# Performance work log

Measured on AMD Instinct MI355X. Metric: run time of the kernel, lower is better.

Reference implementation:

```python
import jax, jax.numpy as jnp
import numpy as np

# Config (matches init_kwargs): range [-32,32]^3, voxel 0.5 -> 128^3 grid; BEV 200x200
PC_LOW = np.array([-32.0, -32.0, -32.0], dtype=np.float32)
PC_HIGH = np.array([32.0, 32.0, 32.0], dtype=np.float32)
VOX = 0.5
G = 128
BEV_H, BEV_W = 200, 200
BN_EPS = 1e-5
STRIDES = [1, 2, 1, 2, 1, 1]


def setup_inputs() -> dict:
    key = jax.random.key(0)
    ks = jax.random.split(key, 10)
    N = 2_000_000
    xyz = jax.random.uniform(ks[0], (N, 3), jnp.float32, minval=-32.0, maxval=32.0)
    inten = jax.random.uniform(ks[1], (N, 1), jnp.float32)
    points = jnp.concatenate([xyz, inten], axis=1)  # (N,4)
    chans = [(32, 4), (64, 32), (64, 64), (128, 64), (128, 128), (256, 128)]
    inp = {"points": points}
    for i, (co, ci) in enumerate(chans):
        fan_in = ci * 27
        inp[f"w{i+1}"] = jax.random.normal(ks[2 + i], (co, ci, 3, 3, 3), jnp.float32) / np.sqrt(fan_in)
        inp[f"g{i+1}"] = jnp.ones((co,), jnp.float32)
        inp[f"b{i+1}"] = jnp.zeros((co,), jnp.float32)
    return inp


def _voxelize(points):
    # range filtering + floor-binning + clamp, faithful to voxelize_points (dense path: scatter-ADD)
    low = jnp.asarray(PC_LOW)
    high = jnp.asarray(PC_HIGH)
    mask = jnp.all((points[:, :3] >= low) & (points[:, :3] <= high), axis=1)
    coords = jnp.floor((points[:, :3] - low) / VOX).astype(jnp.int32)
    coords = jnp.clip(coords, 0, G - 1)
    vals = points * mask[:, None].astype(points.dtype)  # invalid points contribute 0
    # original indexes voxel_grid[:, z, y, x]
    grid = jnp.zeros((G, G, G, 4), points.dtype)
    grid = grid.at[coords[:, 2], coords[:, 1], coords[:, 0]].add(vals)
    return jnp.transpose(grid, (3, 0, 1, 2))  # (4, G, G, G)


def _conv3d(x, w, s):
    # PyTorch Conv3d(k=3, padding=1, stride=s), NCDHW
    return jax.lax.conv_general_dilated(
        x, w, window_strides=(s, s, s), padding=[(1, 1), (1, 1), (1, 1)],
        dimension_numbers=("NCDHW", "OIDHW", "NCDHW"))


def _bn_relu(x, g, b):
    # eval-mode BN: running_mean=0, running_var=1
    scale = (g / jnp.sqrt(1.0 + BN_EPS))[None, :, None, None, None]
    return jax.nn.relu(x * scale + b[None, :, None, None, None])


def reference(points, w1, w2, w3, w4, w5, w6,
              g1, g2, g3, g4, g5, g6,
              b1, b2, b3, b4, b5, b6):
    ws = [w1, w2, w3, w4, w5, w6]
    gs = [g1, g2, g3, g4, g5, g6]
    bs = [b1, b2, b3, b4, b5, b6]
    x = _voxelize(points)[None]  # (1,4,G,G,G)
    for w, g, b, s in zip(ws, gs, bs, STRIDES):
        x = _bn_relu(_conv3d(x, w, s), g, b)
    feat = x[0]  # (256, G/4, G/4, G/4)
    bev = jnp.max(feat, axis=2)  # torch.max(..., dim=2) on (C,D1,D2,D3) -> (C,D1,D3)
    # F.interpolate bilinear align_corners=False == jax.image.resize half-pixel bilinear
    bev = jax.image.resize(bev, (bev.shape[0], BEV_H, BEV_W), method="bilinear")
    return bev
```

## Files before the change

kernel.cpp:

```cpp
#include <hip/hip_runtime.h>
#include <hip/hip_fp16.h>
#include <cstdint>
#include <cstddef>

typedef __attribute__((ext_vector_type(8))) short short8;
typedef __attribute__((ext_vector_type(8))) _Float16 half8;
typedef __attribute__((ext_vector_type(16))) float f32x16;

__device__ __forceinline__ float bf2f(unsigned short u) { return __uint_as_float(((unsigned)u) << 16); }
__device__ __forceinline__ unsigned short f2bf(float f) {
    unsigned u = __float_as_uint(f);
    return (unsigned short)((u + 0x7fffu + ((u >> 16) & 1u)) >> 16);
}
__device__ __forceinline__ void sync_lds() {
    asm volatile("s_waitcnt lgkmcnt(0)\n\ts_barrier" ::: "memory");
}

static constexpr float BN_INV = 0.9999950000374997f;

__global__ __launch_bounds__(256) void voxelize_kernel(const float4* __restrict__ pts,
                                                       __half2* __restrict__ grid, int N) {
    int i = blockIdx.x * 256 + threadIdx.x;
    if (i >= N) return;
    float4 p = pts[i];
    if (p.x < -32.f || p.x > 32.f || p.y < -32.f || p.y > 32.f || p.z < -32.f || p.z > 32.f) return;
    int cx = min(max((int)floorf((p.x + 32.f) * 2.f), 0), 127);
    int cy = min(max((int)floorf((p.y + 32.f) * 2.f), 0), 127);
    int cz = min(max((int)floorf((p.z + 32.f) * 2.f), 0), 127);
    int idx = ((((cz + 1) * 130) + (cy + 1)) * 130 + (cx + 1)) * 2;
    unsafeAtomicAdd(&grid[idx],     __floats2half2_rn(p.x, p.y));
    unsafeAtomicAdd(&grid[idx + 1], __floats2half2_rn(p.z, p.w));
}

__global__ __launch_bounds__(256) void repack_w(const float* __restrict__ w, const float* __restrict__ g,
                                                unsigned short* __restrict__ o, int Co, int CI) {
    int i = blockIdx.x * 256 + threadIdx.x;
    int total = 27 * Co * CI;
    if (i >= total) return;
    int ci = i % CI;
    int t = i / CI;
    int co = t % Co;
    int k = t / Co;
    float v = w[((size_t)(co * CI + ci)) * 27 + k] * g[co] * BN_INV;
    o[i] = f2bf(v);
}
__global__ __launch_bounds__(256) void repack_w1m(const float* __restrict__ w, const float* __restrict__ g,
                                                  unsigned short* __restrict__ o) {
    int i = blockIdx.x * 256 + threadIdx.x;
    if (i >= 9 * 32 * 16) return;
    int k16 = i & 15;
    int co = (i >> 4) & 31;
    int p = i >> 9;
    float v = 0.f;
    if (k16 < 12) {
        int dx = k16 >> 2, ci = k16 & 3;
        int dz = p / 3, dy = p % 3;
        v = w[(co * 4 + ci) * 27 + dz * 9 + dy * 3 + dx] * g[co] * BN_INV;
    }
    o[i] = __half_as_ushort(__float2half(v));
}

__global__ __launch_bounds__(256) void conv1_mfma(
    const unsigned short* __restrict__ in, const unsigned short* __restrict__ wa,
    const float* __restrict__ beta, unsigned short* __restrict__ out,
    int zstart, int r0) {
    const int tid = threadIdx.x;
    const int l31 = tid & 31;
    const int lh = (tid >> 5) & 1;
    const int wv = tid >> 6;
    int v = blockIdx.x * 128 + wv * 32 + l31;
    int x = v & 127;
    int y = (v >> 7) & 127;
    int z = zstart + (v >> 14);

    const unsigned short* base = in + ((z * 130 + y) * 130 + x) * 4 + lh * 8;
    uint2 d0[9], d1[9];
    half8 a[9];
#pragma unroll
    for (int p = 0; p < 9; ++p) {
        int dz = p / 3, dy = p % 3;
        const unsigned short* rp = base + (dz * 130 + dy) * 520;
        d0[p] = *(const uint2*)(rp);
        d1[p] = *(const uint2*)(rp + 4);
        a[p] = *(const half8*)(wa + (p * 32 + l31) * 16 + lh * 8);
    }
    f32x16 acc = {0.f};
#pragma unroll
    for (int p = 0; p < 9; ++p) {
        uint4 braw = {d0[p].x, d0[p].y, d1[p].x, d1[p].y};
        half8 b = *(half8*)&braw;
        acc = __builtin_amdgcn_mfma_f32_32x32x16_f16(a[p], b, acc, 0, 0, 0);
    }
    int r = z - zstart + r0;
    int ob = ((r * 130 + (y + 1)) * 130 + (x + 1)) * 32;
#pragma unroll
    for (int g = 0; g < 4; ++g) {
        int cb = 4 * lh + 8 * g;
        float4 bt = *(const float4*)(beta + cb);
        ushort4 u;
        u.x = f2bf(fmaxf(acc[g * 4 + 0] + bt.x, 0.f));
        u.y = f2bf(fmaxf(acc[g * 4 + 1] + bt.y, 0.f));
        u.z = f2bf(fmaxf(acc[g * 4 + 2] + bt.z, 0.f));
        u.w = f2bf(fmaxf(acc[g * 4 + 3] + bt.w, 0.f));
        *(ushort4*)(out + ob + cb) = u;
    }
}

template <int CI, int KC, int S>
__global__ __launch_bounds__(256) void conv_mfma(
    const unsigned short* __restrict__ in, const unsigned short* __restrict__ wb,
    const float* __restrict__ beta, unsigned short* __restrict__ out,
    int D, int lgD, int Xp, int Xpo, int Co, int zin_base, int v_off) {

    constexpr int KCp = KC + 8;
    constexpr int OPB = KC / 8;
    constexpr int NB = KC / 16;
    constexpr int NA = KC / 32;
    constexpr int NCH = KC / 16;
    constexpr int NCC = CI / KC;
    constexpr int STOT = 27 * NCC;

    __shared__ __align__(16) short sA[2 * 64 * KCp];
    __shared__ __align__(16) short sB[2 * 128 * KCp];

    const int tid = threadIdx.x;
    const int l31 = tid & 31;
    const int lh = (tid >> 5) & 1;
    const int wv = tid >> 6;
    const int co0 = blockIdx.x * 64;

    int bgIdx[NB], blB[NB];
#pragma unroll
    for (int j = 0; j < NB; ++j) {
        int idx = tid + j * 256;
        int vL = idx / OPB;
        int oct = idx - vL * OPB;
        int vg = v_off + blockIdx.y * 128 + vL;
        int x = vg & (D - 1);
        int ry = vg >> lgD;
        int y = ry & (D - 1);
        int z = ry >> lgD;
        bgIdx[j] = ((z * S * Xp + y * S) * Xp + x * S) * CI + oct * 8;
        blB[j] = vL * KCp + oct * 8;
    }
    int agIdx[NA], alA[NA];
#pragma unroll
    for (int j = 0; j < NA; ++j) {
        int idx = tid + j * 256;
        int cA = idx / OPB;
        int oct = idx - cA * OPB;
        agIdx[j] = (co0 + cA) * CI + oct * 8;
        alA[j] = cA * KCp + oct * 8;
    }
    const int bfr = (wv * 32 + l31) * KCp + lh * 8;
    const int afr = l31 * KCp + lh * 8;

    short8 rB[2][NB], rA[2][NA];

    auto loadStage = [&](int s, int r) {
        int k = s / NCC;
        int c0 = (s - k * NCC) * KC;
        int dz = k / 9;
        int rr = k - dz * 9;
        int dy = rr / 3;
        int dx = rr - dy * 3;
        int kb = (((dz - zin_base) * Xp + dy) * Xp + dx) * CI + c0;
        int ka = k * Co * CI + c0;
#pragma unroll
        for (int j = 0; j < NB; ++j) rB[r][j] = *(const short8*)(in + bgIdx[j] + kb);
#pragma unroll
        for (int j = 0; j < NA; ++j) rA[r][j] = *(const short8*)(wb + agIdx[j] + ka);
    };
    auto storeLDS = [&](int r, int buf) {
#pragma unroll
        for (int j = 0; j < NB; ++j) *(short8*)(sB + buf * 128 * KCp + blB[j]) = rB[r][j];
#pragma unroll
        for (int j = 0; j < NA; ++j) *(short8*)(sA + buf * 64 * KCp + alA[j]) = rA[r][j];
    };

    f32x16 acc0 = {0.f}, acc1 = {0.f};

    loadStage(0, 0);
    loadStage(1, 1);
    storeLDS(0, 0);
    sync_lds();

#pragma unroll
    for (int s = 0; s < STOT; ++s) {
        if (s + 2 < STOT) loadStage(s + 2, s & 1);
        const short* pB = sB + (s & 1) * 128 * KCp + bfr;
        const short* pA = sA + (s & 1) * 64 * KCp + afr;
#pragma unroll
        for (int c = 0; c < NCH; ++c) {
            short8 bv = *(const short8*)(pB + c * 16);
            short8 a0 = *(const short8*)(pA + c * 16);
            short8 a1 = *(const short8*)(pA + 32 * KCp + c * 16);
            acc0 = __builtin_amdgcn_mfma_f32_32x32x16_bf16(a0, bv, acc0, 0, 0, 0);
            acc1 = __builtin_amdgcn_mfma_f32_32x32x16_bf16(a1, bv, acc1, 0, 0, 0);
        }
        if (s + 1 < STOT) {
            storeLDS((s + 1) & 1, (s + 1) & 1);
            sync_lds();
        }
    }

    int vg = v_off + blockIdx.y * 128 + wv * 32 + l31;
    int x = vg & (D - 1);
    int ry = vg >> lgD;
    int y = ry & (D - 1);
    int z = ry >> lgD;
    size_t ob = (((size_t)(z + 1) * Xpo + (y + 1)) * Xpo + (x + 1)) * Co + co0;
#pragma unroll
    for (int cot = 0; cot < 2; ++cot) {
        const f32x16& a = cot ? acc1 : acc0;
#pragma unroll
        for (int g = 0; g < 4; ++g) {
            int cb = cot * 32 + 4 * lh + 8 * g;
            float4 bt = *(const float4*)(beta + co0 + cb);
            ushort4 u;
            u.x = f2bf(fmaxf(a[g * 4 + 0] + bt.x, 0.f));
            u.y = f2bf(fmaxf(a[g * 4 + 1] + bt.y, 0.f));
            u.z = f2bf(fmaxf(a[g * 4 + 2] + bt.z, 0.f));
            u.w = f2bf(fmaxf(a[g * 4 + 3] + bt.w, 0.f));
            *(ushort4*)(out + ob + cb) = u;
        }
    }
}

__global__ __launch_bounds__(256) void bev_max_kernel(const unsigned short* __restrict__ feat,
                                                      float* __restrict__ bev) {
    int z = blockIdx.x >> 5;
    int x = blockIdx.x & 31;
    int c = threadIdx.x;
    const unsigned short* p = feat + ((((z + 1) * 34) + 1) * 34 + (x + 1)) * 256 + c;
    float mx = 0.f;
#pragma unroll
    for (int y = 0; y < 32; ++y) mx = fmaxf(mx, bf2f(p[y * 34 * 256]));
    bev[(z * 32 + x) * 256 + c] = mx;
}

__global__ __launch_bounds__(256) void resize_kernel(const float* __restrict__ bev,
                                                     float* __restrict__ out) {
    int i = blockIdx.x * 256 + threadIdx.x;
    if (i >= 256 * 200 * 200) return;
    int ox = i % 200;
    int t = i / 200;
    int oy = t % 200;
    int c = t / 200;
    const float sc = 32.0f / 200.0f;
    float fy = (oy + 0.5f) * sc - 0.5f;
    float fx = (ox + 0.5f) * sc - 0.5f;
    float fy0 = floorf(fy), fx0 = floorf(fx);
    float ty = fy - fy0, tx = fx - fx0;
    int y0 = min(max((int)fy0, 0), 31), y1 = min(max((int)fy0 + 1, 0), 31);
    int x0 = min(max((int)fx0, 0), 31), x1 = min(max((int)fx0 + 1, 0), 31);
    float v00 = bev[(y0 * 32 + x0) * 256 + c], v01 = bev[(y0 * 32 + x1) * 256 + c];
    float v10 = bev[(y1 * 32 + x0) * 256 + c], v11 = bev[(y1 * 32 + x1) * 256 + c];
    float top = v00 + tx * (v01 - v00);
    float bot = v10 + tx * (v11 - v10);
    out[i] = top + ty * (bot - top);
}

extern "C" void kernel_launch(void* const* d_in, const int* in_sizes, int n_in,
                              void* d_out, int out_size, void* d_ws, size_t ws_size,
                              hipStream_t stream) {
    const float* points = (const float*)d_in[0];
    int N = in_sizes[0] / 4;
    const float *W[6], *G[6], *B[6];
    for (int i = 0; i < 6; ++i) {
        W[i] = (const float*)d_in[1 + 3 * i];
        G[i] = (const float*)d_in[2 + 3 * i];
        B[i] = (const float*)d_in[3 + 3 * i];
    }

    char* ws = (char*)d_ws;
    const size_t MiB = 1ull << 20;
    unsigned short* gridH = (unsigned short*)(ws);
    unsigned short* O1s = (unsigned short*)(ws + 18 * MiB);
    unsigned short* O2p = (unsigned short*)(ws + 104 * MiB);
    unsigned short* O3p = (unsigned short*)(ws);
    unsigned short* O4p = (unsigned short*)(ws + 37 * MiB);
    unsigned short* O5p = (unsigned short*)(ws + 48 * MiB);
    unsigned short* O6p = (unsigned short*)(ws + 59 * MiB);
    float* bev = (float*)(ws + 80 * MiB);
    unsigned short* wc1 = (unsigned short*)(ws + 140 * MiB);
    unsigned short* wb2 = (unsigned short*)(ws + 140 * MiB + 16384);
    unsigned short* wb3 = wb2 + 27 * 64 * 32;
    unsigned short* wb4 = wb3 + 27 * 64 * 64;
    unsigned short* wb5 = wb4 + 27 * 128 * 64;
    unsigned short* wb6 = wb5 + 27 * 128 * 128;

    repack_w1m<<<18, 256, 0, stream>>>(W[0], G[0], wc1);
    repack_w<<<216, 256, 0, stream>>>(W[1], G[1], wb2, 64, 32);
    repack_w<<<432, 256, 0, stream>>>(W[2], G[2], wb3, 64, 64);
    repack_w<<<864, 256, 0, stream>>>(W[3], G[3], wb4, 128, 64);
    repack_w<<<1728, 256, 0, stream>>>(W[4], G[4], wb5, 128, 128);
    repack_w<<<3456, 256, 0, stream>>>(W[5], G[5], wb6, 256, 128);

    hipMemsetAsync(gridH, 0, 17576000, stream);
    hipMemsetAsync(O2p, 0, 36799488, stream);
    voxelize_kernel<<<(N + 255) / 256, 256, 0, stream>>>((const float4*)points, (__half2*)gridH, N);

    hipMemsetAsync(O1s, 0, 70304000, stream);
    conv1_mfma<<<8192, 256, 0, stream>>>(gridH, wc1, B[0], O1s, 0, 1);
    conv_mfma<32, 32, 2><<<dim3(1, 1024), 256, 0, stream>>>(O1s, wb2, B[1], O2p, 64, 6, 130, 66, 64, 0, 0);
    conv1_mfma<<<8320, 256, 0, stream>>>(gridH, wc1, B[0], O1s, 63, 0);
    conv_mfma<32, 32, 2><<<dim3(1, 1024), 256, 0, stream>>>(O1s, wb2, B[1], O2p, 64, 6, 130, 66, 64, 64, 131072);

    hipMemsetAsync(O3p, 0, 36799488, stream);
    hipMemsetAsync(O4p, 0, 10061824, stream);
    hipMemsetAsync(O5p, 0, 10061824, stream);
    hipMemsetAsync(O6p, 0, 20123648, stream);

    conv_mfma<64, 64, 1><<<dim3(1, 2048), 256, 0, stream>>>(O2p, wb3, B[2], O3p, 64, 6, 66, 66, 64, 0, 0);
    conv_mfma<64, 64, 2><<<dim3(2, 256), 256, 0, stream>>>(O3p, wb4, B[3], O4p, 32, 5, 66, 34, 128, 0, 0);
    conv_mfma<128, 64, 1><<<dim3(2, 256), 256, 0, stream>>>(O4p, wb5, B[4], O5p, 32, 5, 34, 34, 128, 0, 0);
    conv_mfma<128, 64, 1><<<dim3(4, 256), 256, 0, stream>>>(O5p, wb6, B[5], O6p, 32, 5, 34, 34, 256, 0, 0);

    bev_max_kernel<<<1024, 256, 0, stream>>>(O6p, bev);
    resize_kernel<<<40000, 256, 0, stream>>>(bev, (float*)d_out);
}
```

Baseline: 759.3 us.

## Stage input rows with dx halo in LDS, read weights from global, zero only halos

Each conv block now loads a full input row strip (with the 3-wide x halo) per (dz,dy) tap into LDS once, and reuses it across the three dx taps. This cuts the pipeline from 27 stages to 9 per channel chunk and removes redundant input loads. Weight fragments are now read straight from global memory (L1/L2) instead of being staged through LDS. Full-buffer memsets of the padded activations are replaced by kernels that zero only the halo faces, and one layer's KC is changed. The risk is that direct global weight loads now sit on the MFMA critical path.

```diff
diff --git a/kernel.cpp b/kernel.cpp
--- a/kernel.cpp
+++ b/kernel.cpp
@@ -30,6 +30,46 @@
     int idx = ((((cz + 1) * 130) + (cy + 1)) * 130 + (cx + 1)) * 2;
     unsafeAtomicAdd(&grid[idx],     __floats2half2_rn(p.x, p.y));
     unsafeAtomicAdd(&grid[idx + 1], __floats2half2_rn(p.z, p.w));
+}
+
+__global__ __launch_bounds__(256) void zero_halo(unsigned short* __restrict__ buf, int Xp, int C8, int total) {
+    int i = blockIdx.x * 256 + threadIdx.x;
+    if (i >= total) return;
+    int c8 = i % C8; int t = i / C8;
+    int b = t % Xp; t /= Xp;
+    int a = t % Xp; int f = t / Xp;
+    int X = Xp - 1;
+    int z, y, x;
+    switch (f) {
+        case 0: z = 0; y = a; x = b; break;
+        case 1: z = X; y = a; x = b; break;
+        case 2: z = a; y = 0; x = b; break;
+        case 3: z = a; y = X; x = b; break;
+        case 4: z = a; y = b; x = 0; break;
+        default: z = a; y = b; x = X; break;
+    }
+    size_t o = ((((size_t)z * Xp + y) * Xp) + x) * (C8 * 8) + c8 * 8;
+    short8 zz = {};
+    *(short8*)(buf + o) = zz;
+}
+__global__ __launch_bounds__(256) void zero_halo_yx(unsigned short* __restrict__ buf, int Zn, int Xp,
+                                                    int C8, int total) {
+    int i = blockIdx.x * 256 + threadIdx.x;
+    if (i >= total) return;
+    int c8 = i % C8; int t = i / C8;
+    int b = t % Xp; t /= Xp;
+    int z = t % Zn; int f = t / Zn;
+    int X = Xp - 1;
+    int y, x;
+    switch (f) {
+        case 0: y = 0; x = b; break;
+        case 1: y = X; x = b; break;
+        case 2: y = b; x = 0; break;
+        default: y = b; x = X; break;
+    }
+    size_t o = ((((size_t)z * Xp + y) * Xp) + x) * (C8 * 8) + c8 * 8;
+    short8 zz = {};
+    *(short8*)(buf + o) = zz;
 }
 
 __global__ __launch_bounds__(256) void repack_w(const float* __restrict__ w, const float* __restrict__ g,
@@ -106,76 +146,84 @@
     }
 }
 
-template <int CI, int KC, int S>
+template <int CI, int KC, int S, int D>
 __global__ __launch_bounds__(256) void conv_mfma(
     const unsigned short* __restrict__ in, const unsigned short* __restrict__ wb,
     const float* __restrict__ beta, unsigned short* __restrict__ out,
-    int D, int lgD, int Xp, int Xpo, int Co, int zin_base, int v_off) {
-
+    int Xp, int Xpo, int Co, int zin_base, int v_off) {
+
+    constexpr int lgD = (D == 64) ? 6 : 5;
+    constexpr int NR = 128 / D;
+    constexpr int Lx = (D - 1) * S + 3;
     constexpr int KCp = KC + 8;
-    constexpr int OPB = KC / 8;
-    constexpr int NB = KC / 16;
-    constexpr int NA = KC / 32;
+    constexpr int OPV = KC / 8;
+    constexpr int OPR = Lx * OPV;
+    constexpr int OCT = NR * OPR;
+    constexpr int NB4 = OCT >> 8;
+    constexpr int TAIL = OCT - NB4 * 256;
     constexpr int NCH = KC / 16;
     constexpr int NCC = CI / KC;
-    constexpr int STOT = 27 * NCC;
-
-    __shared__ __align__(16) short sA[2 * 64 * KCp];
-    __shared__ __align__(16) short sB[2 * 128 * KCp];
+    constexpr int STOT = 9 * NCC;
+    constexpr int RT = NR * Lx;
+
+    __shared__ __align__(16) short sB[2 * RT * KCp];
 
     const int tid = threadIdx.x;
     const int l31 = tid & 31;
     const int lh = (tid >> 5) & 1;
     const int wv = tid >> 6;
+    const int coh = (wv & 1) * 32;
+    const int vh = (wv >> 1) * 64;
     const int co0 = blockIdx.x * 64;
 
-    int bgIdx[NB], blB[NB];
-#pragma unroll
-    for (int j = 0; j < NB; ++j) {
-        int idx = tid + j * 256;
-        int vL = idx / OPB;
-        int oct = idx - vL * OPB;
-        int vg = v_off + blockIdx.y * 128 + vL;
-        int x = vg & (D - 1);
-        int ry = vg >> lgD;
-        int y = ry & (D - 1);
-        int z = ry >> lgD;
-        bgIdx[j] = ((z * S * Xp + y * S) * Xp + x * S) * CI + oct * 8;
-        blB[j] = vL * KCp + oct * 8;
-    }
-    int agIdx[NA], alA[NA];
-#pragma unroll
-    for (int j = 0; j < NA; ++j) {
-        int idx = tid + j * 256;
-        int cA = idx / OPB;
-        int oct = idx - cA * OPB;
-        agIdx[j] = (co0 + cA) * CI + oct * 8;
-        alA[j] = cA * KCp + oct * 8;
-    }
-    const int bfr = (wv * 32 + l31) * KCp + lh * 8;
-    const int afr = l31 * KCp + lh * 8;
-
-    short8 rB[2][NB], rA[2][NA];
-
-    auto loadStage = [&](int s, int r) {
-        int k = s / NCC;
-        int c0 = (s - k * NCC) * KC;
-        int dz = k / 9;
-        int rr = k - dz * 9;
-        int dy = rr / 3;
-        int dx = rr - dy * 3;
-        int kb = (((dz - zin_base) * Xp + dy) * Xp + dx) * CI + c0;
-        int ka = k * Co * CI + c0;
-#pragma unroll
-        for (int j = 0; j < NB; ++j) rB[r][j] = *(const short8*)(in + bgIdx[j] + kb);
-#pragma unroll
-        for (int j = 0; j < NA; ++j) rA[r][j] = *(const short8*)(wb + agIdx[j] + ka);
+    const int v0 = v_off + blockIdx.y * 128;
+    const int z0 = v0 >> (2 * lgD);
+    const int y0 = (v0 >> lgD) & (D - 1);
+
+    int srow[NB4 + 1], sgi[NB4 + 1], sli[NB4 + 1];
+#pragma unroll
+    for (int j = 0; j <= NB4; ++j) {
+        int o = tid + j * 256;
+        int r = o / OPR;
+        int rem = o - r * OPR;
+        int i = rem / OPV;
+        int ov = rem - i * OPV;
+        srow[j] = r;
+        sgi[j] = i * CI + ov * 8;
+        sli[j] = (r * Lx + i) * KCp + ov * 8;
+    }
+    int bfr[2];
+#pragma unroll
+    for (int vt = 0; vt < 2; ++vt) {
+        int lv = vh + vt * 32 + l31;
+        int p = lv & (D - 1);
+        int r = lv >> lgD;
+        bfr[vt] = (r * Lx + p * S) * KCp + lh * 8;
+    }
+    const int aw = (co0 + coh + l31) * CI + lh * 8;
+
+    short8 rB[2][NB4 + 1];
+
+    auto loadStage = [&](int s, int slot) {
+        int k9 = s / NCC;
+        int c0 = (s - k9 * NCC) * KC;
+        int dz = k9 / 3, dy = k9 - dz * 3;
+        int zrow = z0 * S + dz - zin_base;
+#pragma unroll
+        for (int j = 0; j < NB4; ++j) {
+            int rb = ((zrow * Xp + (y0 + srow[j]) * S + dy) * Xp) * CI + c0;
+            rB[slot][j] = *(const short8*)(in + rb + sgi[j]);
+        }
+        if (TAIL && tid < TAIL) {
+            int rb = ((zrow * Xp + (y0 + srow[NB4]) * S + dy) * Xp) * CI + c0;
+            rB[slot][NB4] = *(const short8*)(in + rb + sgi[NB4]);
+        }
     };
-    auto storeLDS = [&](int r, int buf) {
-#pragma unroll
-        for (int j = 0; j < NB; ++j) *(short8*)(sB + buf * 128 * KCp + blB[j]) = rB[r][j];
-#pragma unroll
-        for (int j = 0; j < NA; ++j) *(short8*)(sA + buf * 64 * KCp + alA[j]) = rA[r][j];
+    auto storeLDS = [&](int slot, int buf) {
+        short* d = sB + buf * RT * KCp;
+#pragma unroll
+        for (int j = 0; j < NB4; ++j) *(short8*)(d + sli[j]) = rB[slot][j];
+        if (TAIL && tid < TAIL) *(short8*)(d + sli[NB4]) = rB[slot][NB4];
     };
 
     f32x16 acc0 = {0.f}, acc1 = {0.f};
@@ -188,15 +236,22 @@
 #pragma unroll
     for (int s = 0; s < STOT; ++s) {
         if (s + 2 < STOT) loadStage(s + 2, s & 1);
-        const short* pB = sB + (s & 1) * 128 * KCp + bfr;
-        const short* pA = sA + (s & 1) * 64 * KCp + afr;
-#pragma unroll
-        for (int c = 0; c < NCH; ++c) {
-            short8 bv = *(const short8*)(pB + c * 16);
-            short8 a0 = *(const short8*)(pA + c * 16);
-            short8 a1 = *(const short8*)(pA + 32 * KCp + c * 16);
-            acc0 = __builtin_amdgcn_mfma_f32_32x32x16_bf16(a0, bv, acc0, 0, 0, 0);
-            acc1 = __builtin_amdgcn_mfma_f32_32x32x16_bf16(a1, bv, acc1, 0, 0, 0);
+        {
+            int k9 = s / NCC;
+            int c0 = (s - k9 * NCC) * KC;
+            const short* pB = sB + (s & 1) * RT * KCp;
+            size_t kwb = (size_t)(k9 * 3) * Co * CI + c0;
+#pragma unroll
+            for (int dx = 0; dx < 3; ++dx) {
+#pragma unroll
+                for (int c = 0; c < NCH; ++c) {
+                    short8 av = *(const short8*)(wb + kwb + (size_t)dx * Co * CI + aw + c * 16);
+                    short8 b0 = *(const short8*)(pB + bfr[0] + dx * KCp + c * 16);
+                    short8 b1 = *(const short8*)(pB + bfr[1] + dx * KCp + c * 16);
+                    acc0 = __builtin_amdgcn_mfma_f32_32x32x16_bf16(av, b0, acc0, 0, 0, 0);
+                    acc1 = __builtin_amdgcn_mfma_f32_32x32x16_bf16(av, b1, acc1, 0, 0, 0);
+                }
+            }
         }
         if (s + 1 < STOT) {
             storeLDS((s + 1) & 1, (s + 1) & 1);
@@ -204,19 +259,17 @@
         }
     }
 
-    int vg = v_off + blockIdx.y * 128 + wv * 32 + l31;
-    int x = vg & (D - 1);
-    int ry = vg >> lgD;
-    int y = ry & (D - 1);
-    int z = ry >> lgD;
-    size_t ob = (((size_t)(z + 1) * Xpo + (y + 1)) * Xpo + (x + 1)) * Co + co0;
-#pragma unroll
-    for (int cot = 0; cot < 2; ++cot) {
-        const f32x16& a = cot ? acc1 : acc0;
+#pragma unroll
+    for (int vt = 0; vt < 2; ++vt) {
+        const f32x16& a = vt ? acc1 : acc0;
+        int lv = vh + vt * 32 + l31;
+        int x = lv & (D - 1);
+        int yv = y0 + (lv >> lgD);
+        size_t ob = (((size_t)(z0 + 1) * Xpo + (yv + 1)) * Xpo + (x + 1)) * Co + co0 + coh;
 #pragma unroll
         for (int g = 0; g < 4; ++g) {
-            int cb = cot * 32 + 4 * lh + 8 * g;
-            float4 bt = *(const float4*)(beta + co0 + cb);
+            int cb = 4 * lh + 8 * g;
+            float4 bt = *(const float4*)(beta + co0 + coh + cb);
             ushort4 u;
             u.x = f2bf(fmaxf(a[g * 4 + 0] + bt.x, 0.f));
             u.y = f2bf(fmaxf(a[g * 4 + 1] + bt.y, 0.f));
@@ -276,7 +329,7 @@
     char* ws = (char*)d_ws;
     const size_t MiB = 1ull << 20;
     unsigned short* gridH = (unsigned short*)(ws);
-    unsigned short* O1s = (unsigned short*)(ws + 18 * MiB);
+    unsigned short* O1s = (unsigned short*)(ws + 36 * MiB);
     unsigned short* O2p = (unsigned short*)(ws + 104 * MiB);
     unsigned short* O3p = (unsigned short*)(ws);
     unsigned short* O4p = (unsigned short*)(ws + 37 * MiB);
@@ -298,24 +351,26 @@
     repack_w<<<3456, 256, 0, stream>>>(W[5], G[5], wb6, 256, 128);
 
     hipMemsetAsync(gridH, 0, 17576000, stream);
-    hipMemsetAsync(O2p, 0, 36799488, stream);
+    zero_halo<<<817, 256, 0, stream>>>(O2p, 66, 8, 6 * 66 * 66 * 8);
     voxelize_kernel<<<(N + 255) / 256, 256, 0, stream>>>((const float4*)points, (__half2*)gridH, N);
 
-    hipMemsetAsync(O1s, 0, 70304000, stream);
+    hipMemsetAsync(O1s, 0, 1081600, stream);
+    zero_halo_yx<<<529, 256, 0, stream>>>(O1s, 65, 130, 4, 4 * 65 * 130 * 4);
+
     conv1_mfma<<<8192, 256, 0, stream>>>(gridH, wc1, B[0], O1s, 0, 1);
-    conv_mfma<32, 32, 2><<<dim3(1, 1024), 256, 0, stream>>>(O1s, wb2, B[1], O2p, 64, 6, 130, 66, 64, 0, 0);
+    conv_mfma<32, 32, 2, 64><<<dim3(1, 1024), 256, 0, stream>>>(O1s, wb2, B[1], O2p, 130, 66, 64, 0, 0);
     conv1_mfma<<<8320, 256, 0, stream>>>(gridH, wc1, B[0], O1s, 63, 0);
-    conv_mfma<32, 32, 2><<<dim3(1, 1024), 256, 0, stream>>>(O1s, wb2, B[1], O2p, 64, 6, 130, 66, 64, 64, 131072);
-
-    hipMemsetAsync(O3p, 0, 36799488, stream);
-    hipMemsetAsync(O4p, 0, 10061824, stream);
-    hipMemsetAsync(O5p, 0, 10061824, stream);
-    hipMemsetAsync(O6p, 0, 20123648, stream);
-
-    conv_mfma<64, 64, 1><<<dim3(1, 2048), 256, 0, stream>>>(O2p, wb3, B[2], O3p, 64, 6, 66, 66, 64, 0, 0);
-    conv_mfma<64, 64, 2><<<dim3(2, 256), 256, 0, stream>>>(O3p, wb4, B[3], O4p, 32, 5, 66, 34, 128, 0, 0);
-    conv_mfma<128, 64, 1><<<dim3(2, 256), 256, 0, stream>>>(O4p, wb5, B[4], O5p, 32, 5, 34, 34, 128, 0, 0);
-    conv_mfma<128, 64, 1><<<dim3(4, 256), 256, 0, stream>>>(O5p, wb6, B[5], O6p, 32, 5, 34, 34, 256, 0, 0);
+    conv_mfma<32, 32, 2, 64><<<dim3(1, 1024), 256, 0, stream>>>(O1s, wb2, B[1], O2p, 130, 66, 64, 64, 131072);
+
+    zero_halo<<<817, 256, 0, stream>>>(O3p, 66, 8, 6 * 66 * 66 * 8);
+    zero_halo<<<434, 256, 0, stream>>>(O4p, 34, 16, 6 * 34 * 34 * 16);
+    zero_halo<<<434, 256, 0, stream>>>(O5p, 34, 16, 6 * 34 * 34 * 16);
+    zero_halo<<<868, 256, 0, stream>>>(O6p, 34, 32, 6 * 34 * 34 * 32);
+
+    conv_mfma<64, 64, 1, 64><<<dim3(1, 2048), 256, 0, stream>>>(O2p, wb3, B[2], O3p, 66, 66, 64, 0, 0);
+    conv_mfma<64, 32, 2, 32><<<dim3(2, 256), 256, 0, stream>>>(O3p, wb4, B[3], O4p, 66, 34, 128, 0, 0);
+    conv_mfma<128, 64, 1, 32><<<dim3(2, 256), 256, 0, stream>>>(O4p, wb5, B[4], O5p, 34, 34, 128, 0, 0);
+    conv_mfma<128, 64, 1, 32><<<dim3(4, 256), 256, 0, stream>>>(O5p, wb6, B[5], O6p, 34, 34, 256, 0, 0);
 
     bev_max_kernel<<<1024, 256, 0, stream>>>(O6p, bev);
     resize_kernel<<<40000, 256, 0, stream>>>(bev, (float*)d_out);
```

New measurement: 906.2 us. 1.19x slower.
